# Kernel tuning notes

Hardware: AMD Instinct MI355X
Metric: run time of the kernel (lower is better)

The kernel has to match this reference:

```python
import jax, jax.numpy as jnp
import numpy as np


def _euler_zyx(R):
    # R: [B,3,3]; standard zyx (Tait-Bryan) extraction, non-singular branch
    sy = jnp.sqrt(R[:, 0, 0] ** 2 + R[:, 1, 0] ** 2)
    x = jnp.arctan2(R[:, 2, 1], R[:, 2, 2])
    y = jnp.arctan2(-R[:, 2, 0], sy)
    z = jnp.arctan2(R[:, 1, 0], R[:, 0, 0])
    return jnp.stack([x, y, z], axis=1)  # [B,3]


def setup_inputs() -> dict:
    key = jax.random.key(0)
    k1, k2, k3, k4 = jax.random.split(key, 4)
    B, D, N = 8, 128, 3072
    return {
        "src_embedding": jax.random.normal(k1, (B, D, N), dtype=jnp.float32),
        "tgt_embedding": jax.random.normal(k2, (B, D, N), dtype=jnp.float32),
        "src": jax.random.normal(k3, (B, 3, N), dtype=jnp.float32),
        "tgt": jax.random.normal(k4, (B, 3, N), dtype=jnp.float32),
    }


def reference(src_embedding, tgt_embedding, src, tgt):
    B = src.shape[0]
    d_k = src_embedding.shape[1]
    # attention scores over target points: [B, N, M]
    scores = jnp.einsum("bdn,bdm->bnm", src_embedding, tgt_embedding) / jnp.sqrt(
        jnp.asarray(d_k, src_embedding.dtype)
    )
    scores = jax.nn.softmax(scores, axis=2)
    # soft correspondences: tgt @ scores^T -> [B, 3, N]
    src_corr = jnp.einsum("bdm,bnm->bdn", tgt, scores)
    src_mean = src.mean(axis=2, keepdims=True)          # [B,3,1]
    corr_mean = src_corr.mean(axis=2, keepdims=True)    # [B,3,1]
    src_c = src - src_mean
    corr_c = src_corr - corr_mean
    # cross-covariance H: [B,3,3]
    H = jnp.einsum("bin,bjn->bij", src_c, corr_c)
    u, s, vh = jnp.linalg.svd(H)
    v = jnp.swapaxes(vh, 1, 2)                          # torch.svd returns V
    ut = jnp.swapaxes(u, 1, 2)
    r = v @ ut
    det = jnp.linalg.det(r)                             # [B]
    sign = jnp.where(det < 0, -1.0, 1.0)                # reflection fix
    ones = jnp.ones_like(sign)
    col_scale = jnp.stack([ones, ones, sign], axis=-1)[:, None, :]  # scale last col of V
    v = v * col_scale
    R = v @ ut                                          # [B,3,3]
    t = (-R @ src_mean + corr_mean).reshape(B, 3)
    mus = _euler_zyx(R)
    return (R, t, mus)
```

## Files before the change

kernel.cpp:

```cpp
#include <hip/hip_runtime.h>
#include <hip/hip_bf16.h>
#include <math.h>

#define BN 8
#define DEMB 128
#define NP 3072
#define MSPLIT 8
#define MRANGE (NP / MSPLIT)
#define NCHUNK (MRANGE / 64)
#define NBLK 256
#define NWAVE 64
#define ESTRIDE 138

#define QT_ELEMS ((size_t)BN * NP * DEMB)

typedef __attribute__((ext_vector_type(8))) short short8;
typedef __attribute__((ext_vector_type(4))) float f32x4;

__device__ inline float fast_exp2(float x) {
#if __has_builtin(__builtin_amdgcn_exp2f)
    return __builtin_amdgcn_exp2f(x);
#else
    return __expf(x * 0.6931471805599453f);
#endif
}

#define PSTRIDE 132

__global__ __launch_bounds__(256) void k_prep(const float* __restrict__ qe,
                                              const float* __restrict__ te,
                                              ushort* __restrict__ qT,
                                              ushort* __restrict__ eT)
{
    __shared__ ushort lds[4][16 * PSTRIDE];

    const int bid = blockIdx.x;
    const int t   = bid & 1;
    const int b   = (bid >> 1) & 7;
    const int nb  = bid >> 4;

    const float* src = (t ? te : qe) + (size_t)b * DEMB * NP;
    ushort*      dst = (t ? eT : qT) + (size_t)b * NP * DEMB;

    const int w    = threadIdx.x >> 6;
    const int lane = threadIdx.x & 63;
    const int n0   = nb * 64 + w * 16;

#pragma unroll
    for (int p = 0; p < 8; ++p) {
        const int d  = p * 16 + (lane >> 2);
        const int nn = (lane & 3) * 4;
        const f32x4 v = *(const f32x4*)(src + (size_t)d * NP + n0 + nn);
#pragma unroll
        for (int k = 0; k < 4; ++k) {
            __hip_bfloat16 h = __float2bfloat16(v[k]);
            lds[w][(nn + k) * PSTRIDE + d] = *reinterpret_cast<ushort*>(&h);
        }
    }
    __syncthreads();

#pragma unroll
    for (int q = 0; q < 8; ++q) {
        const int flat = q * 256 + lane * 4;
        const int n = flat >> 7;
        const int d = flat & 127;
        uint2 vv;
        vv.x = *(const uint*)&lds[w][n * PSTRIDE + d];
        vv.y = *(const uint*)&lds[w][n * PSTRIDE + d + 2];
        *(uint2*)(dst + ((size_t)(n0 + n)) * DEMB + d) = vv;
    }
}

__global__ __launch_bounds__(256, 2) void k_attn(const ushort* __restrict__ qT,
                                                 const ushort* __restrict__ eT,
                                                 const float* __restrict__ tgt,
                                                 float4* __restrict__ part)
{
    __shared__ ushort esm[2][64][ESTRIDE];
    __shared__ float  tbuf[3][MRANGE];

    const int bid  = blockIdx.x;
    const int b    = bid & 7;
    const int r    = bid >> 3;
    const int nblk = r % 12;
    const int ms   = r / 12;

    const int wid  = threadIdx.x >> 6;
    const int lane = threadIdx.x & 63;
    const int g    = lane >> 4;
    const int c16  = lane & 15;

    const int nw = nblk * NBLK + wid * NWAVE;
    const ushort* qb = qT + (size_t)b * NP * DEMB;
    const ushort* eb = eT + (size_t)b * NP * DEMB;
    const float*  tp = tgt + (size_t)b * 3 * NP;
    const int m_base = ms * MRANGE;

    for (int j = threadIdx.x; j < 3 * MRANGE; j += 256) {
        const int c = j / MRANGE, jm = j % MRANGE;
        tbuf[c][jm] = tp[c * NP + m_base + jm];
    }

    short8 bq[4][4];
#pragma unroll
    for (int ns = 0; ns < 4; ++ns)
#pragma unroll
        for (int kf = 0; kf < 4; ++kf)
            bq[ns][kf] = *(const short8*)(qb + (size_t)(nw + ns * 16 + c16) * DEMB
                                          + kf * 32 + g * 8);

    float o[4][4];
#pragma unroll
    for (int ns = 0; ns < 4; ++ns)
        o[ns][0] = o[ns][1] = o[ns][2] = o[ns][3] = 0.f;

    const float scale2 = 0.12752962736873462f;

    const int row_l = wid * 16 + c16;
    const ushort* arow = eb + (size_t)(m_base + row_l) * DEMB + g * 8;

    for (int mc = 0; mc < NCHUNK; ++mc) {
        const ushort* asrc = arow + (size_t)mc * 64 * DEMB;
        const short8 a0 = *(const short8*)(asrc);
        const short8 a1 = *(const short8*)(asrc + 32);
        const short8 a2 = *(const short8*)(asrc + 64);
        const short8 a3 = *(const short8*)(asrc + 96);

        __syncthreads();
        {
            ushort* erw = &esm[mc & 1][row_l][0];
            *(short8*)(erw + (0 * 4 + g) * 8) = a0;
            *(short8*)(erw + (1 * 4 + g) * 8) = a1;
            *(short8*)(erw + (2 * 4 + g) * 8) = a2;
            *(short8*)(erw + (3 * 4 + g) * 8) = a3;
        }
        __syncthreads();

#pragma unroll
        for (int msub = 0; msub < 4; ++msub) {
            const ushort* erow = &esm[mc & 1][msub * 16 + c16][0];
            const short8 e0 = *(const short8*)(erow + (0 * 4 + g) * 8);
            const short8 e1 = *(const short8*)(erow + (1 * 4 + g) * 8);
            const short8 e2 = *(const short8*)(erow + (2 * 4 + g) * 8);
            const short8 e3 = *(const short8*)(erow + (3 * 4 + g) * 8);

            f32x4 c[4];
#pragma unroll
            for (int ns = 0; ns < 4; ++ns) {
                c[ns] = (f32x4){0.f, 0.f, 0.f, 0.f};
                c[ns] = __builtin_amdgcn_mfma_f32_16x16x32_bf16(e0, bq[ns][0], c[ns], 0, 0, 0);
                c[ns] = __builtin_amdgcn_mfma_f32_16x16x32_bf16(e1, bq[ns][1], c[ns], 0, 0, 0);
                c[ns] = __builtin_amdgcn_mfma_f32_16x16x32_bf16(e2, bq[ns][2], c[ns], 0, 0, 0);
                c[ns] = __builtin_amdgcn_mfma_f32_16x16x32_bf16(e3, bq[ns][3], c[ns], 0, 0, 0);
            }

            const int mloc = mc * 64 + msub * 16 + g * 4;
            const f32x4 t0 = *(const f32x4*)&tbuf[0][mloc];
            const f32x4 t1 = *(const f32x4*)&tbuf[1][mloc];
            const f32x4 t2 = *(const f32x4*)&tbuf[2][mloc];

#pragma unroll
            for (int ns = 0; ns < 4; ++ns) {
#pragma unroll
                for (int rr = 0; rr < 4; ++rr) {
                    const float p = fast_exp2(c[ns][rr] * scale2);
                    o[ns][3] += p;
                    o[ns][0] = fmaf(p, t0[rr], o[ns][0]);
                    o[ns][1] = fmaf(p, t1[rr], o[ns][1]);
                    o[ns][2] = fmaf(p, t2[rr], o[ns][2]);
                }
            }
        }
    }

#pragma unroll
    for (int ns = 0; ns < 4; ++ns) {
#pragma unroll
        for (int v = 0; v < 4; ++v) {
            o[ns][v] += __shfl_xor(o[ns][v], 16);
            o[ns][v] += __shfl_xor(o[ns][v], 32);
        }
        if (g == 0) {
            const int n = nw + ns * 16 + c16;
            float4 pv;
            pv.x = o[ns][0]; pv.y = o[ns][1]; pv.z = o[ns][2]; pv.w = o[ns][3];
            part[((size_t)ms * BN + b) * NP + n] = pv;
        }
    }
}

__global__ __launch_bounds__(256) void k_final(const float* __restrict__ src,
                                               const float4* __restrict__ part,
                                               float* __restrict__ out)
{
    const int b = blockIdx.x;
    const float* sp = src + (size_t)b * 3 * NP;

    double acc[15];
#pragma unroll
    for (int v = 0; v < 15; ++v) acc[v] = 0.0;

    for (int n = threadIdx.x; n < NP; n += 256) {
        float o0 = 0.f, o1 = 0.f, o2 = 0.f, l = 0.f;
#pragma unroll
        for (int s = 0; s < MSPLIT; ++s) {
            const float4 pp = part[((size_t)s * BN + b) * NP + n];
            o0 += pp.x; o1 += pp.y; o2 += pp.z; l += pp.w;
        }
        const double inv = 1.0 / (double)l;
        const double y0 = o0 * inv, y1 = o1 * inv, y2 = o2 * inv;
        const double x0 = sp[n], x1 = sp[NP + n], x2 = sp[2 * NP + n];
        acc[0] += x0; acc[1] += x1; acc[2] += x2;
        acc[3] += y0; acc[4] += y1; acc[5] += y2;
        acc[6]  += x0 * y0; acc[7]  += x0 * y1; acc[8]  += x0 * y2;
        acc[9]  += x1 * y0; acc[10] += x1 * y1; acc[11] += x1 * y2;
        acc[12] += x2 * y0; acc[13] += x2 * y1; acc[14] += x2 * y2;
    }

    const int wid = threadIdx.x >> 6, lane = threadIdx.x & 63;
#pragma unroll
    for (int v = 0; v < 15; ++v)
#pragma unroll
        for (int mask = 32; mask >= 1; mask >>= 1)
            acc[v] += __shfl_xor(acc[v], mask);

    __shared__ double red[4][15];
    if (lane == 0) {
#pragma unroll
        for (int v = 0; v < 15; ++v) red[wid][v] = acc[v];
    }
    __syncthreads();
    if (threadIdx.x != 0) return;

    double t15[15];
#pragma unroll
    for (int v = 0; v < 15; ++v)
        t15[v] = red[0][v] + red[1][v] + red[2][v] + red[3][v];

    const double invN = 1.0 / NP;
    const double mx[3] = {t15[0] * invN, t15[1] * invN, t15[2] * invN};
    const double my[3] = {t15[3] * invN, t15[4] * invN, t15[5] * invN};
    double H[3][3];
#pragma unroll
    for (int i = 0; i < 3; ++i)
#pragma unroll
        for (int j = 0; j < 3; ++j)
            H[i][j] = t15[6 + i * 3 + j] - (double)NP * mx[i] * my[j];

    double A[3][3], V[3][3];
#pragma unroll
    for (int i = 0; i < 3; ++i)
#pragma unroll
        for (int j = 0; j < 3; ++j) {
            A[i][j] = H[0][i] * H[0][j] + H[1][i] * H[1][j] + H[2][i] * H[2][j];
            V[i][j] = (i == j) ? 1.0 : 0.0;
        }

    for (int sweep = 0; sweep < 12; ++sweep) {
        const int pqs[3][2] = {{0, 1}, {0, 2}, {1, 2}};
        for (int k = 0; k < 3; ++k) {
            const int p = pqs[k][0], q = pqs[k][1];
            const double apq = A[p][q];
            if (apq * apq <= 1e-24 * (A[p][p] * A[p][p] + A[q][q] * A[q][q]))
                continue;
            const double theta = (A[q][q] - A[p][p]) / (2.0 * apq);
            const double tj = (theta >= 0 ? 1.0 : -1.0) /
                              (fabs(theta) + sqrt(theta * theta + 1.0));
            const double c = 1.0 / sqrt(tj * tj + 1.0);
            const double s = tj * c;
            for (int i = 0; i < 3; ++i) {
                const double aip = A[i][p], aiq = A[i][q];
                A[i][p] = c * aip - s * aiq;
                A[i][q] = s * aip + c * aiq;
            }
            for (int i = 0; i < 3; ++i) {
                const double api = A[p][i], aqi = A[q][i];
                A[p][i] = c * api - s * aqi;
                A[q][i] = s * api + c * aqi;
            }
            for (int i = 0; i < 3; ++i) {
                const double vip = V[i][p], viq = V[i][q];
                V[i][p] = c * vip - s * viq;
                V[i][q] = s * vip + c * viq;
            }
        }
    }

    double lam[3] = {A[0][0], A[1][1], A[2][2]};
    int ord[3] = {0, 1, 2};
    for (int i = 0; i < 2; ++i)
        for (int j = i + 1; j < 3; ++j)
            if (lam[ord[j]] > lam[ord[i]]) { int t = ord[i]; ord[i] = ord[j]; ord[j] = t; }

    double Vs[3][3], sv[3];
    for (int j = 0; j < 3; ++j) {
        sv[j] = sqrt(fmax(lam[ord[j]], 0.0));
        for (int i = 0; i < 3; ++i) Vs[i][j] = V[i][ord[j]];
    }
    double U[3][3];
    for (int j = 0; j < 3; ++j) {
        const double h0 = H[0][0] * Vs[0][j] + H[0][1] * Vs[1][j] + H[0][2] * Vs[2][j];
        const double h1 = H[1][0] * Vs[0][j] + H[1][1] * Vs[1][j] + H[1][2] * Vs[2][j];
        const double h2 = H[2][0] * Vs[0][j] + H[2][1] * Vs[1][j] + H[2][2] * Vs[2][j];
        const double inv = 1.0 / fmax(sv[j], 1e-300);
        U[0][j] = h0 * inv; U[1][j] = h1 * inv; U[2][j] = h2 * inv;
    }

    double R[3][3];
    for (int i = 0; i < 3; ++i)
        for (int j = 0; j < 3; ++j)
            R[i][j] = Vs[i][0] * U[j][0] + Vs[i][1] * U[j][1] + Vs[i][2] * U[j][2];
    const double det =
        R[0][0] * (R[1][1] * R[2][2] - R[1][2] * R[2][1]) -
        R[0][1] * (R[1][0] * R[2][2] - R[1][2] * R[2][0]) +
        R[0][2] * (R[1][0] * R[2][1] - R[1][1] * R[2][0]);
    if (det < 0.0) {
        Vs[0][2] = -Vs[0][2]; Vs[1][2] = -Vs[1][2]; Vs[2][2] = -Vs[2][2];
        for (int i = 0; i < 3; ++i)
            for (int j = 0; j < 3; ++j)
                R[i][j] = Vs[i][0] * U[j][0] + Vs[i][1] * U[j][1] + Vs[i][2] * U[j][2];
    }

    double tvec[3];
    for (int i = 0; i < 3; ++i)
        tvec[i] = -(R[i][0] * mx[0] + R[i][1] * mx[1] + R[i][2] * mx[2]) + my[i];

    const double ex = atan2(R[2][1], R[2][2]);
    const double syv = sqrt(R[0][0] * R[0][0] + R[1][0] * R[1][0]);
    const double ey = atan2(-R[2][0], syv);
    const double ez = atan2(R[1][0], R[0][0]);

    for (int i = 0; i < 3; ++i)
        for (int j = 0; j < 3; ++j)
            out[b * 9 + i * 3 + j] = (float)R[i][j];
    out[72 + b * 3 + 0] = (float)tvec[0];
    out[72 + b * 3 + 1] = (float)tvec[1];
    out[72 + b * 3 + 2] = (float)tvec[2];
    out[96 + b * 3 + 0] = (float)ex;
    out[96 + b * 3 + 1] = (float)ey;
    out[96 + b * 3 + 2] = (float)ez;
}

extern "C" void kernel_launch(void* const* d_in, const int* in_sizes, int n_in,
                              void* d_out, int out_size, void* d_ws, size_t ws_size,
                              hipStream_t stream) {
    const float* qe  = (const float*)d_in[0];
    const float* te  = (const float*)d_in[1];
    const float* src = (const float*)d_in[2];
    const float* tgt = (const float*)d_in[3];
    float* out = (float*)d_out;

    ushort* qT   = (ushort*)d_ws;
    ushort* eT   = qT + QT_ELEMS;
    float4* part = (float4*)(eT + QT_ELEMS);

    k_prep<<<768, 256, 0, stream>>>(qe, te, qT, eT);
    k_attn<<<768, 256, 0, stream>>>(qT, eT, tgt, part);
    k_final<<<BN, 256, 0, stream>>>(src, part, out);
}
```

Before: 86.81 us.

## Prefetch next E chunk into registers and single-buffer LDS tile

Global loads for the next 64-row embedding chunk are issued right after the LDS store barrier, so their latency overlaps the MFMA work on the current chunk instead of stalling at the top of each iteration. The LDS tile drops from double to single buffering, which the two barriers per iteration make safe. The launch bounds no longer request two blocks per CU. This changes register allocation and may raise register pressure through the extra prefetch registers, which could affect occupancy.

```diff
diff --git a/kernel.cpp b/kernel.cpp
--- a/kernel.cpp
+++ b/kernel.cpp
@@ -71,12 +71,12 @@
     }
 }
 
-__global__ __launch_bounds__(256, 2) void k_attn(const ushort* __restrict__ qT,
-                                                 const ushort* __restrict__ eT,
-                                                 const float* __restrict__ tgt,
-                                                 float4* __restrict__ part)
+__global__ __launch_bounds__(256) void k_attn(const ushort* __restrict__ qT,
+                                              const ushort* __restrict__ eT,
+                                              const float* __restrict__ tgt,
+                                              float4* __restrict__ part)
 {
-    __shared__ ushort esm[2][64][ESTRIDE];
+    __shared__ ushort esm[64][ESTRIDE];
     __shared__ float  tbuf[3][MRANGE];
 
     const int bid  = blockIdx.x;
@@ -119,26 +119,33 @@
     const int row_l = wid * 16 + c16;
     const ushort* arow = eb + (size_t)(m_base + row_l) * DEMB + g * 8;
 
+    short8 pa0 = *(const short8*)(arow);
+    short8 pa1 = *(const short8*)(arow + 32);
+    short8 pa2 = *(const short8*)(arow + 64);
+    short8 pa3 = *(const short8*)(arow + 96);
+
     for (int mc = 0; mc < NCHUNK; ++mc) {
-        const ushort* asrc = arow + (size_t)mc * 64 * DEMB;
-        const short8 a0 = *(const short8*)(asrc);
-        const short8 a1 = *(const short8*)(asrc + 32);
-        const short8 a2 = *(const short8*)(asrc + 64);
-        const short8 a3 = *(const short8*)(asrc + 96);
-
         __syncthreads();
         {
-            ushort* erw = &esm[mc & 1][row_l][0];
-            *(short8*)(erw + (0 * 4 + g) * 8) = a0;
-            *(short8*)(erw + (1 * 4 + g) * 8) = a1;
-            *(short8*)(erw + (2 * 4 + g) * 8) = a2;
-            *(short8*)(erw + (3 * 4 + g) * 8) = a3;
+            ushort* erw = &esm[row_l][0];
+            *(short8*)(erw + (0 * 4 + g) * 8) = pa0;
+            *(short8*)(erw + (1 * 4 + g) * 8) = pa1;
+            *(short8*)(erw + (2 * 4 + g) * 8) = pa2;
+            *(short8*)(erw + (3 * 4 + g) * 8) = pa3;
         }
         __syncthreads();
 
+        if (mc + 1 < NCHUNK) {
+            const ushort* asrc = arow + (size_t)(mc + 1) * 64 * DEMB;
+            pa0 = *(const short8*)(asrc);
+            pa1 = *(const short8*)(asrc + 32);
+            pa2 = *(const short8*)(asrc + 64);
+            pa3 = *(const short8*)(asrc + 96);
+        }
+
 #pragma unroll
         for (int msub = 0; msub < 4; ++msub) {
-            const ushort* erow = &esm[mc & 1][msub * 16 + c16][0];
+            const ushort* erow = &esm[msub * 16 + c16][0];
             const short8 e0 = *(const short8*)(erow + (0 * 4 + g) * 8);
             const short8 e1 = *(const short8*)(erow + (1 * 4 + g) * 8);
             const short8 e2 = *(const short8*)(erow + (2 * 4 + g) * 8);
```

Result: no change. 87.07 us (+0.3%).
